# Optimization experiments

Measured on AMD Instinct MI355X. Metric: run time of the kernel, lower is better.

## Reference

```python
import jax, jax.numpy as jnp
from jax import lax
import numpy as np

COST_CLASS, COST_BBOX, COST_GIOU = 2.0, 5.0, 2.0
ALPHA, GAMMA, OTA_K = 0.25, 2.0, 5
EXPANDED_STRIDES = 32.0
DEG = 180.0 / np.pi


def _make_corners(key, prefix):
    k1, k2, k3, k4, k5 = jax.random.split(key, 5)
    cx = jax.random.uniform(k1, prefix, minval=0.0, maxval=512.0)
    cy = jax.random.uniform(k2, prefix, minval=0.0, maxval=512.0)
    w = jax.random.uniform(k3, prefix, minval=8.0, maxval=128.0)
    h = jax.random.uniform(k4, prefix, minval=8.0, maxval=128.0)
    ang = jax.random.uniform(k5, prefix, minval=0.0, maxval=np.pi)
    offs = jnp.array([[-0.5, -0.5], [0.5, -0.5], [0.5, 0.5], [-0.5, 0.5]], jnp.float32)
    wh = jnp.stack([w, h], -1)[..., None, :]          # [..., 1, 2]
    pts = offs * wh                                    # [..., 4, 2]
    c, s = jnp.cos(ang)[..., None], jnp.sin(ang)[..., None]
    rx = pts[..., 0] * c - pts[..., 1] * s + cx[..., None]
    ry = pts[..., 0] * s + pts[..., 1] * c + cy[..., None]
    return jnp.stack([rx, ry], -1).reshape(prefix + (8,))


def setup_inputs() -> dict:
    key = jax.random.key(0)
    k1, k2, k3, k4 = jax.random.split(key, 4)
    B, Q, G, C = 16, 4096, 128, 80
    return {
        "pred_logits": jax.random.normal(k1, (B, Q, C), jnp.float32),
        "pred_boxes": _make_corners(k2, (B, Q)),
        "gt_boxes": _make_corners(k3, (B, G)),
        "gt_labels": jax.random.randint(k4, (B, G), 0, C),
    }


def corners_to_cxcywha(c):  # [N,8] -> [N,5]
    xc = (c[:, 0] + c[:, 2] + c[:, 4] + c[:, 6]) / 4
    yc = (c[:, 1] + c[:, 3] + c[:, 5] + c[:, 7]) / 4
    w = jnp.sqrt((c[:, 0] - c[:, 2]) ** 2 + (c[:, 1] - c[:, 3]) ** 2)
    h = jnp.sqrt((c[:, 2] - c[:, 4]) ** 2 + (c[:, 3] - c[:, 5]) ** 2)
    ang = jnp.arctan2(c[:, 3] - c[:, 1], c[:, 2] - c[:, 0]) * DEG
    return jnp.stack([xc, yc, w, h, ang], 1)


def _aabb(b5):
    cx, cy, w, h = b5[:, 0], b5[:, 1], b5[:, 2], b5[:, 3]
    return jnp.stack([cx - w / 2, cy - h / 2, cx + w / 2, cy + h / 2], 1)


def pairwise_iou(b1, b2):
    a, b = _aabb(b1), _aabb(b2)
    lt = jnp.maximum(a[:, None, :2], b[None, :, :2])
    rb = jnp.minimum(a[:, None, 2:], b[None, :, 2:])
    wh = jnp.clip(rb - lt, 0.0)
    inter = wh[..., 0] * wh[..., 1]
    area1 = (a[:, 2] - a[:, 0]) * (a[:, 3] - a[:, 1])
    area2 = (b[:, 2] - b[:, 0]) * (b[:, 3] - b[:, 1])
    return inter / (area1[:, None] + area2[None, :] - inter + 1e-8)


def pairwise_diou(b1, b2):
    iou = pairwise_iou(b1, b2)
    a, b = _aabb(b1), _aabb(b2)
    enc = jnp.maximum(a[:, None, 2:], b[None, :, 2:]) - jnp.minimum(a[:, None, :2], b[None, :, :2])
    c2 = (enc ** 2).sum(-1) + 1e-8
    d2 = ((b1[:, None, :2] - b2[None, :, :2]) ** 2).sum(-1)
    return iou - d2 / c2


def get_in_boxes_info(boxes, gts):
    bc = boxes.reshape(-1, 4, 2).mean(1)   # [Q,2]
    gp = gts.reshape(-1, 4, 2)             # [G,4,2]
    gc = gp.mean(1)                        # [G,2]
    cdist = jnp.sqrt(((bc[:, None] - gc[None]) ** 2).sum(-1))  # [Q,G]
    v1 = gp[:, 1] - gp[:, 0]
    v2 = gp[:, 2] - gp[:, 0]
    gt_area = jnp.abs(v1[:, 0] * v2[:, 1] - v1[:, 1] * v2[:, 0]) / 2
    diag = jnp.sqrt(((gp.max(1) - gp.min(1)) ** 2).sum(-1))
    radius = diag / EXPANDED_STRIDES
    in_boxes = cdist <= (gt_area / radius)[None, :]
    in_centers = cdist <= radius[None, :]
    return in_boxes.any(1), in_boxes & in_centers


def _dedup(cost, m):
    multi = m.sum(1) > 1
    onehot = jax.nn.one_hot(jnp.argmin(cost, 1), cost.shape[1], dtype=m.dtype)
    return jnp.where(multi[:, None], onehot, m)


def _match_single(logits, pboxes, gboxes, glabels):
    Q, G = pboxes.shape[0], gboxes.shape[0]
    prob = jax.nn.sigmoid(logits)
    fg_mask, _ = get_in_boxes_info(pboxes, gboxes)
    p5, g5 = corners_to_cxcywha(pboxes), corners_to_cxcywha(gboxes)
    ious = pairwise_iou(p5, g5)
    neg = (1 - ALPHA) * prob ** GAMMA * -jnp.log(1 - prob + 1e-8)
    pos = ALPHA * (1 - prob) ** GAMMA * -jnp.log(prob + 1e-8)
    cost_class = (pos - neg)[:, glabels]                         # [Q,G]
    cost_bbox = jnp.abs(pboxes[:, None] - gboxes[None]).sum(-1)  # L1 cdist on corners
    cost_giou = -pairwise_diou(p5, g5)
    # NB: source has `+ self.cost_giou * -cost_giou`, i.e. +w*diou; replicated verbatim.
    cost = COST_BBOX * cost_bbox + COST_CLASS * cost_class + COST_GIOU * (-cost_giou)
    cost = cost + 10000.0 * (~fg_mask)[:, None].astype(cost.dtype)
    # dynamic-k: sum of top OTA_K ious per gt, truncated to int, min 1
    topk = lax.top_k(ious.T, OTA_K)[0]                 # [G, k]
    dyn_k = jnp.clip(topk.sum(-1).astype(jnp.int32), 1, Q)
    ranks = jnp.argsort(jnp.argsort(cost, axis=0), axis=0)  # ascending-cost rank per column
    matching = (ranks < dyn_k[None, :]).astype(cost.dtype)
    matching = _dedup(cost, matching)
    # ensure every gt matched (bounded replication of the while loop)
    def cond(carry):
        c, m, it = carry
        return jnp.any(m.sum(0) == 0) & (it < G)
    def body(carry):
        c, m, it = carry
        c = c + 100000.0 * (m.sum(1) > 0)[:, None].astype(c.dtype)
        unm = m.sum(0) == 0
        amin = jnp.argmin(c, 0)                          # [G]
        hit = (jnp.arange(Q)[:, None] == amin[None, :]) & unm[None, :]
        m = jnp.where(hit, 1.0, m)
        m = _dedup(c, m)
        return (c, m, it + 1)
    _, matching, _ = lax.while_loop(cond, body, (cost, matching, jnp.int32(0)))
    return matching, cost, ious


def reference(pred_logits, pred_boxes, gt_boxes, gt_labels):
    return jax.vmap(_match_single)(pred_logits, pred_boxes, gt_boxes, gt_labels)
```

## Files before the change

### kernel.cpp

```cpp
#include <hip/hip_runtime.h>
#include <cstdint>
#include <cstddef>

#define B_ 16
#define Q_ 4096
#define G_ 128
#define C_ 80
#define QCHUNK 16
#define NCH (Q_ / QCHUNK)

typedef unsigned long long u64;
#define U64MAX 0xffffffffffffffffull

__device__ __forceinline__ u64 packkey(float v, int q) {
    unsigned int bts = __float_as_uint(v);
    if (bts == 0x80000000u) bts = 0u;
    bts = (bts & 0x80000000u) ? ~bts : (bts | 0x80000000u);
    return ((u64)bts << 32) | (unsigned int)q;
}

__device__ __forceinline__ u64 umin64(u64 a, u64 b) { return a < b ? a : b; }
__device__ __forceinline__ u64 umax64(u64 a, u64 b) { return a > b ? a : b; }

__device__ __forceinline__ void merge5_desc(
    float& a0, float& a1, float& a2, float& a3, float& a4,
    float b0, float b1, float b2, float b3, float b4)
{
    const float r0 = fmaxf(a0, b0);
    const float r1 = fmaxf(fmaxf(a1, b1), fminf(a0, b0));
    const float r2 = fmaxf(fmaxf(a2, b2), fmaxf(fminf(a0, b1), fminf(a1, b0)));
    const float r3 = fmaxf(fmaxf(a3, b3),
                     fmaxf(fminf(a0, b2), fmaxf(fminf(a1, b1), fminf(a2, b0))));
    const float r4 = fmaxf(fmaxf(a4, b4),
                     fmaxf(fmaxf(fminf(a0, b3), fminf(a3, b0)),
                           fmaxf(fminf(a1, b2), fminf(a2, b1))));
    a0 = r0; a1 = r1; a2 = r2; a3 = r3; a4 = r4;
}

__device__ __forceinline__ void merge5_asc(
    u64& a0, u64& a1, u64& a2, u64& a3, u64& a4,
    u64 b0, u64 b1, u64 b2, u64 b3, u64 b4)
{
    const u64 r0 = umin64(a0, b0);
    const u64 r1 = umin64(umin64(a1, b1), umax64(a0, b0));
    const u64 r2 = umin64(umin64(a2, b2), umin64(umax64(a0, b1), umax64(a1, b0)));
    const u64 r3 = umin64(umin64(a3, b3),
                   umin64(umax64(a0, b2), umin64(umax64(a1, b1), umax64(a2, b0))));
    const u64 r4 = umin64(umin64(a4, b4),
                   umin64(umin64(umax64(a0, b3), umax64(a3, b0)),
                          umin64(umax64(a1, b2), umax64(a2, b1))));
    a0 = r0; a1 = r1; a2 = r2; a3 = r3; a4 = r4;
}

__device__ __forceinline__ float focal_cost(float x) {
    float p;
    if (x >= 0.f) { const float e = expf(-x); p = 1.f / (1.f + e); }
    else          { const float e = expf(x);  p = e / (1.f + e); }
    const float pos = 0.25f * (1.f - p) * (1.f - p) * (-logf(p + 1e-8f));
    const float neg = 0.75f * p * p * (-logf(1.f - p + 1e-8f));
    return pos - neg;
}

__global__ __launch_bounds__(256) void fused_cost_kernel(
    const float* __restrict__ logits,
    const float* __restrict__ pboxes,
    const float* __restrict__ gboxes,
    const int*   __restrict__ glabels,
    float* __restrict__ out_cost,
    float* __restrict__ out_iou,
    float* __restrict__ costT,
    float* __restrict__ piou,
    u64*   __restrict__ pcost,
    int*   __restrict__ ramin)
{
    const int tid = threadIdx.x;
    const int g   = tid & 127;
    const int qh  = tid >> 7;
    const int ci  = blockIdx.x, b = blockIdx.y;
    const int q0  = ci * QCHUNK;

    __shared__ float pq[QCHUNK][16];
    __shared__ int   fgf[QCHUNK];
    __shared__ __align__(16) char lk_buf[5120];
    __shared__ float ctile[QCHUNK][G_ + 1];
    __shared__ float phalf[G_][5];
    float* lbuf = (float*)lk_buf;
    u64 (*khalf)[5] = (u64(*)[5])lk_buf;

    const float4* gb4 = (const float4*)(gboxes + ((size_t)b * G_ + g) * 8);
    const float4 gA = gb4[0], gB = gb4[1];
    const float g0 = gA.x, g1 = gA.y, g2 = gA.z, g3 = gA.w;
    const float g4 = gB.x, g5 = gB.y, g6 = gB.z, g7 = gB.w;
    const float gxc = (g0 + g2 + g4 + g6) * 0.25f;
    const float gyc = (g1 + g3 + g5 + g7) * 0.25f;
    const float gw = sqrtf((g0 - g2) * (g0 - g2) + (g1 - g3) * (g1 - g3));
    const float gh = sqrtf((g2 - g4) * (g2 - g4) + (g3 - g5) * (g3 - g5));
    const float gax0 = gxc - gw * 0.5f, gay0 = gyc - gh * 0.5f;
    const float gax1 = gxc + gw * 0.5f, gay1 = gyc + gh * 0.5f;
    const float garea = (gax1 - gax0) * (gay1 - gay0);
    const float v1x = g2 - g0, v1y = g3 - g1, v2x = g4 - g0, v2y = g5 - g1;
    const float gt_area = fabsf(v1x * v2y - v1y * v2x) * 0.5f;
    const float mxx = fmaxf(fmaxf(g0, g2), fmaxf(g4, g6));
    const float mnx = fminf(fminf(g0, g2), fminf(g4, g6));
    const float mxy = fmaxf(fmaxf(g1, g3), fmaxf(g5, g7));
    const float mny = fminf(fminf(g1, g3), fminf(g5, g7));
    const float dgx = mxx - mnx, dgy = mxy - mny;
    const float radius = sqrtf(dgx * dgx + dgy * dgy) / 32.0f;
    const float thresh = gt_area / radius;
    const int lab = glabels[b * G_ + g];

    if (tid < 32) {
        const float4 v = ((const float4*)(pboxes + ((size_t)b * Q_ + q0) * 8))[tid];
        *(float4*)&pq[tid >> 1][(tid & 1) * 4] = v;
    }
    __syncthreads();
    if (tid < QCHUNK) {
        const float* pr = pq[tid];
        const float p0 = pr[0], p1 = pr[1], p2 = pr[2], p3 = pr[3];
        const float p4 = pr[4], p5v = pr[5], p6 = pr[6], p7 = pr[7];
        const float pxc = (p0 + p2 + p4 + p6) * 0.25f;
        const float pyc = (p1 + p3 + p5v + p7) * 0.25f;
        const float pw = sqrtf((p0 - p2) * (p0 - p2) + (p1 - p3) * (p1 - p3));
        const float ph = sqrtf((p2 - p4) * (p2 - p4) + (p3 - p5v) * (p3 - p5v));
        pq[tid][8]  = pxc;
        pq[tid][9]  = pyc;
        pq[tid][10] = pxc - pw * 0.5f;
        pq[tid][11] = pyc - ph * 0.5f;
        pq[tid][12] = pxc + pw * 0.5f;
        pq[tid][13] = pyc + ph * 0.5f;
        pq[tid][14] = pw * ph;
        fgf[tid] = 0;
    }
    __syncthreads();
    for (int j = tid; j < QCHUNK * 80; j += 256)
        lbuf[j] = focal_cost(logits[((size_t)b * Q_ + q0) * 80 + j]);

    const int lane0 = ((tid & 63) == 0);
    for (int i = 0; i < QCHUNK / 2; ++i) {
        const int ql = 2 * i + qh;
        const float dx = pq[ql][8] - gxc, dy = pq[ql][9] - gyc;
        const int in = sqrtf(dx * dx + dy * dy) <= thresh;
        const int anyin = __any(in);
        if (anyin && lane0) fgf[ql] = 1;
    }
    __syncthreads();

    float t0 = -1e38f, t1 = -1e38f, t2 = -1e38f, t3 = -1e38f, t4 = -1e38f;
    u64 k0 = U64MAX, k1 = U64MAX, k2 = U64MAX, k3 = U64MAX, k4 = U64MAX;

    #pragma unroll
    for (int jj = 0; jj < 8; ++jj) {
        const int qls = 2 * jj + qh;
        const int q   = q0 + qls;
        const float4 prA = *(const float4*)&pq[qls][0];
        const float4 prB = *(const float4*)&pq[qls][4];
        const float4 prC = *(const float4*)&pq[qls][8];
        const float4 prD = *(const float4*)&pq[qls][12];
        const float p0 = prA.x, p1 = prA.y, p2 = prA.z, p3 = prA.w;
        const float p4 = prB.x, p5v = prB.y, p6 = prB.z, p7 = prB.w;
        const float pxc = prC.x, pyc = prC.y;
        const float pax0 = prC.z, pay0 = prC.w, pax1 = prD.x, pay1 = prD.y;
        const float parea = prD.z;

        const float l1 = fabsf(p0 - g0) + fabsf(p1 - g1) + fabsf(p2 - g2)
                       + fabsf(p3 - g3) + fabsf(p4 - g4) + fabsf(p5v - g5)
                       + fabsf(p6 - g6) + fabsf(p7 - g7);

        const float ltx = fmaxf(pax0, gax0), lty = fmaxf(pay0, gay0);
        const float rbx = fminf(pax1, gax1), rby = fminf(pay1, gay1);
        const float iw = fmaxf(rbx - ltx, 0.f), ih = fmaxf(rby - lty, 0.f);
        const float inter = iw * ih;
        const float iou = inter / (parea + garea - inter + 1e-8f);

        const float ew = fmaxf(pax1, gax1) - fminf(pax0, gax0);
        const float eh = fmaxf(pay1, gay1) - fminf(pay0, gay0);
        const float cc2 = ew * ew + eh * eh + 1e-8f;
        const float dx = pxc - gxc, dy = pyc - gyc;
        const float diou = iou - (dx * dx + dy * dy) / cc2;

        const float cclass = lbuf[qls * 80 + lab];
        const float cost = 5.f * l1 + 2.f * cclass + 2.f * diou
                         + (fgf[qls] ? 0.f : 10000.f);

        const size_t o = ((size_t)b * Q_ + q) * G_ + g;
        out_cost[o] = cost;
        out_iou[o]  = iou;
        ctile[qls][g] = cost;

        if (iou > t4) {
            if (iou > t0)      { t4 = t3; t3 = t2; t2 = t1; t1 = t0; t0 = iou; }
            else if (iou > t1) { t4 = t3; t3 = t2; t2 = t1; t1 = iou; }
            else if (iou > t2) { t4 = t3; t3 = t2; t2 = iou; }
            else if (iou > t3) { t4 = t3; t3 = iou; }
            else               { t4 = iou; }
        }
        const u64 kk = packkey(cost, q);
        if (kk < k4) {
            if (kk < k0)      { k4 = k3; k3 = k2; k2 = k1; k1 = k0; k0 = kk; }
            else if (kk < k1) { k4 = k3; k3 = k2; k2 = k1; k1 = kk; }
            else if (kk < k2) { k4 = k3; k3 = k2; k2 = kk; }
            else if (kk < k3) { k4 = k3; k3 = kk; }
            else              { k4 = kk; }
        }
    }
    __syncthreads();

    for (int t = tid; t < QCHUNK * G_ / 4; t += 256) {
        const int gg = t >> 2;
        const int k  = (t & 3) << 2;
        float4 o;
        o.x = ctile[k + 0][gg]; o.y = ctile[k + 1][gg];
        o.z = ctile[k + 2][gg]; o.w = ctile[k + 3][gg];
        *(float4*)&costT[((size_t)b * G_ + gg) * Q_ + q0 + k] = o;
    }

    {
        const int qls  = tid >> 4;
        const int part = tid & 15;
        float v = 1e38f; int mg = 0x7fffffff;
        #pragma unroll
        for (int j = 0; j < 8; ++j) {
            const int gg = part + 16 * j;
            const float c = ctile[qls][gg];
            if (c < v || (c == v && gg < mg)) { v = c; mg = gg; }
        }
        #pragma unroll
        for (int off = 1; off < 16; off <<= 1) {
            const float ov = __shfl_xor(v, off);
            const int   og = __shfl_xor(mg, off);
            if (ov < v || (ov == v && og < mg)) { v = ov; mg = og; }
        }
        if (part == 0) ramin[b * Q_ + q0 + qls] = mg;
    }

    if (qh == 1) {
        phalf[g][0] = t0; phalf[g][1] = t1; phalf[g][2] = t2;
        phalf[g][3] = t3; phalf[g][4] = t4;
        khalf[g][0] = k0; khalf[g][1] = k1; khalf[g][2] = k2;
        khalf[g][3] = k3; khalf[g][4] = k4;
    }
    __syncthreads();
    if (qh == 0) {
        merge5_desc(t0, t1, t2, t3, t4,
                    phalf[g][0], phalf[g][1], phalf[g][2], phalf[g][3], phalf[g][4]);
        merge5_asc(k0, k1, k2, k3, k4,
                   khalf[g][0], khalf[g][1], khalf[g][2], khalf[g][3], khalf[g][4]);
        const size_t pbase = (((size_t)b * G_ + g) * NCH + ci) * 5;
        piou[pbase + 0] = t0; piou[pbase + 1] = t1; piou[pbase + 2] = t2;
        piou[pbase + 3] = t3; piou[pbase + 4] = t4;
        pcost[pbase + 0] = k0; pcost[pbase + 1] = k1; pcost[pbase + 2] = k2;
        pcost[pbase + 3] = k3; pcost[pbase + 4] = k4;
    }
}

__global__ __launch_bounds__(256) void dynk_scatter_kernel(
    const u64*   __restrict__ pcost,
    const float* __restrict__ piou,
    u64* __restrict__ cand,
    int* __restrict__ cnt,
    int* __restrict__ gsel)
{
    const int col = blockIdx.x;
    const int b = col >> 7, g = col & 127;
    const int tid = threadIdx.x;
    const int wv = tid >> 6, ln = tid & 63;

    __shared__ u64   wl[4][5];
    __shared__ float il[4][5];

    const size_t base = (size_t)col * (NCH * 5) + (size_t)tid * 5;

    u64 k0 = pcost[base + 0], k1 = pcost[base + 1], k2 = pcost[base + 2],
        k3 = pcost[base + 3], k4 = pcost[base + 4];
    float t0 = piou[base + 0], t1 = piou[base + 1], t2 = piou[base + 2],
          t3 = piou[base + 3], t4 = piou[base + 4];

    #pragma unroll
    for (int off = 1; off < 64; off <<= 1) {
        merge5_asc(k0, k1, k2, k3, k4,
                   __shfl_xor(k0, off), __shfl_xor(k1, off), __shfl_xor(k2, off),
                   __shfl_xor(k3, off), __shfl_xor(k4, off));
        merge5_desc(t0, t1, t2, t3, t4,
                    __shfl_xor(t0, off), __shfl_xor(t1, off), __shfl_xor(t2, off),
                    __shfl_xor(t3, off), __shfl_xor(t4, off));
    }
    if (ln == 0) {
        wl[wv][0] = k0; wl[wv][1] = k1; wl[wv][2] = k2; wl[wv][3] = k3; wl[wv][4] = k4;
        il[wv][0] = t0; il[wv][1] = t1; il[wv][2] = t2; il[wv][3] = t3; il[wv][4] = t4;
    }
    __syncthreads();

    if (tid == 0) {
        u64 f0 = wl[0][0], f1 = wl[0][1], f2 = wl[0][2], f3 = wl[0][3], f4 = wl[0][4];
        merge5_asc(f0, f1, f2, f3, f4, wl[1][0], wl[1][1], wl[1][2], wl[1][3], wl[1][4]);
        merge5_asc(f0, f1, f2, f3, f4, wl[2][0], wl[2][1], wl[2][2], wl[2][3], wl[2][4]);
        merge5_asc(f0, f1, f2, f3, f4, wl[3][0], wl[3][1], wl[3][2], wl[3][3], wl[3][4]);
        float s0 = il[0][0], s1 = il[0][1], s2 = il[0][2], s3 = il[0][3], s4 = il[0][4];
        merge5_desc(s0, s1, s2, s3, s4, il[1][0], il[1][1], il[1][2], il[1][3], il[1][4]);
        merge5_desc(s0, s1, s2, s3, s4, il[2][0], il[2][1], il[2][2], il[2][3], il[2][4]);
        merge5_desc(s0, s1, s2, s3, s4, il[3][0], il[3][1], il[3][2], il[3][3], il[3][4]);

        cand[(size_t)col * 5 + 0] = f0;
        cand[(size_t)col * 5 + 1] = f1;
        cand[(size_t)col * 5 + 2] = f2;
        cand[(size_t)col * 5 + 3] = f3;
        cand[(size_t)col * 5 + 4] = f4;

        const float s = s0 + s1 + s2 + s3 + s4;
        int dynk = (int)s;
        if (dynk < 1) dynk = 1;
        if (dynk > 5) dynk = 5;
        const u64 ks[5] = {f0, f1, f2, f3, f4};
        #pragma unroll
        for (int i = 0; i < 5; ++i) {
            if (i < dynk) {
                const int q = (int)(ks[i] & 0xffffffffu);
                atomicAdd(&cnt[b * Q_ + q], 1);
                gsel[b * Q_ + q] = g;
            }
        }
    }
}

__global__ __launch_bounds__(256) void loop_kernel(
    const float* __restrict__ costT,
    const int* __restrict__ cnt,
    const int* __restrict__ gsel,
    const int* __restrict__ ramin,
    const u64* __restrict__ cand,
    int* __restrict__ rmatch_final)
{
    const int b = blockIdx.x, tid = threadIdx.x;
    const int wv = tid >> 6, ln = tid & 63;

    __shared__ short rmatch[Q_];
    __shared__ unsigned char s_ra[Q_];
    __shared__ int newh[Q_];
    __shared__ unsigned char newg[Q_];
    __shared__ u64 scand[G_][5];
    __shared__ int ptrs[G_], col_cnt[G_], unm_list[G_], prop[G_], fb_slot[G_], touched[G_];
    __shared__ int n_unm, n_fb, n_touch;

    for (int q = tid; q < Q_; q += 256) {
        const int c  = cnt[b * Q_ + q];
        const int ra = ramin[b * Q_ + q];
        s_ra[q] = (unsigned char)ra;
        newh[q] = 0;
        rmatch[q] = (c == 0) ? (short)-1
                             : (c == 1 ? (short)gsel[b * Q_ + q] : (short)ra);
    }
    if (tid < G_) { col_cnt[tid] = 0; ptrs[tid] = 0; }
    for (int i = tid; i < G_ * 5; i += 256)
        scand[i / 5][i % 5] = cand[(size_t)b * G_ * 5 + i];
    __syncthreads();
    for (int q = tid; q < Q_; q += 256)
        if (rmatch[q] >= 0) atomicAdd(&col_cnt[rmatch[q]], 1);
    __syncthreads();

    for (int it = 0; it < G_; ++it) {
        if (tid == 0) { n_unm = 0; n_fb = 0; n_touch = 0; }
        __syncthreads();
        if (tid < G_ && col_cnt[tid] == 0)
            unm_list[atomicAdd(&n_unm, 1)] = tid;
        __syncthreads();
        const int nu = n_unm;
        if (nu == 0) break;

        if (tid < nu) {
            const int g = unm_list[tid];
            int p = ptrs[g];
            int q = -1;
            while (p < 5) {
                const int cq = (int)(scand[g][p] & 0xffffffffu);
                if (rmatch[cq] < 0) { q = cq; break; }
                ++p;
            }
            ptrs[g] = p;
            prop[tid] = q;
            if (q < 0) fb_slot[atomicAdd(&n_fb, 1)] = tid;
        }
        __syncthreads();

        const int nf = n_fb;
        for (int i = wv; i < nf; i += 4) {
            const int slot = fb_slot[i];
            const int g = unm_list[slot];
            const float4* colp = (const float4*)(costT + ((size_t)b * G_ + g) * Q_);
            u64 k0 = U64MAX, k1 = U64MAX, k2 = U64MAX, k3 = U64MAX, k4 = U64MAX;
            #pragma unroll 4
            for (int s = 0; s < Q_ / 256; ++s) {
                const int idx = ln + s * 64;
                const float4 c4 = colp[idx];
                const int qb = idx * 4;
                const float vv[4] = {c4.x, c4.y, c4.z, c4.w};
                #pragma unroll
                for (int j = 0; j < 4; ++j) {
                    if (rmatch[qb + j] < 0) {
                        const u64 kk = packkey(vv[j], qb + j);
                        if (kk < k4) {
                            if (kk < k0)      { k4 = k3; k3 = k2; k2 = k1; k1 = k0; k0 = kk; }
                            else if (kk < k1) { k4 = k3; k3 = k2; k2 = k1; k1 = kk; }
                            else if (kk < k2) { k4 = k3; k3 = k2; k2 = kk; }
                            else if (kk < k3) { k4 = k3; k3 = kk; }
                            else              { k4 = kk; }
                        }
                    }
                }
            }
            #pragma unroll
            for (int off = 1; off < 64; off <<= 1) {
                merge5_asc(k0, k1, k2, k3, k4,
                           __shfl_xor(k0, off), __shfl_xor(k1, off), __shfl_xor(k2, off),
                           __shfl_xor(k3, off), __shfl_xor(k4, off));
            }
            if (ln == 0) {
                scand[g][0] = k0; scand[g][1] = k1; scand[g][2] = k2;
                scand[g][3] = k3; scand[g][4] = k4;
                ptrs[g] = 0;
                prop[slot] = (int)(k0 & 0xffffffffu);
            }
        }
        __syncthreads();

        if (tid < nu) {
            const int q = prop[tid];
            newg[q] = (unsigned char)unm_list[tid];
            if (atomicAdd(&newh[q], 1) == 0)
                touched[atomicAdd(&n_touch, 1)] = q;
        }
        __syncthreads();

        const int nt = n_touch;
        if (tid < nt) {
            const int q = touched[tid];
            const int nh = newh[q];
            const int gg = (nh == 1) ? (int)newg[q] : (int)s_ra[q];
            rmatch[q] = (short)gg;
            atomicAdd(&col_cnt[gg], 1);
            newh[q] = 0;
        }
        __syncthreads();
    }

    for (int q = tid; q < Q_; q += 256)
        rmatch_final[b * Q_ + q] = rmatch[q];
}

__global__ __launch_bounds__(256) void expand_kernel(
    const int* __restrict__ rmatch_final, float* __restrict__ out_match)
{
    const int idx = blockIdx.x * 256 + threadIdx.x;
    const int row = idx >> 5;
    const int gb  = (idx & 31) << 2;
    const int rm  = rmatch_final[row];
    float4 o;
    o.x = (rm == gb)     ? 1.f : 0.f;
    o.y = (rm == gb + 1) ? 1.f : 0.f;
    o.z = (rm == gb + 2) ? 1.f : 0.f;
    o.w = (rm == gb + 3) ? 1.f : 0.f;
    ((float4*)out_match)[idx] = o;
}

extern "C" void kernel_launch(void* const* d_in, const int* in_sizes, int n_in,
                              void* d_out, int out_size, void* d_ws, size_t ws_size,
                              hipStream_t stream) {
    const float* logits  = (const float*)d_in[0];
    const float* pboxes  = (const float*)d_in[1];
    const float* gboxes  = (const float*)d_in[2];
    const int*   glabels = (const int*)d_in[3];

    float* out = (float*)d_out;
    const size_t BQG = (size_t)B_ * Q_ * G_;
    float* out_match = out;
    float* out_cost  = out + BQG;
    float* out_iou   = out + 2 * BQG;

    char* ws = (char*)d_ws;
    size_t off = 0;
    float* costT  = (float*)(ws + off); off += (size_t)B_ * G_ * Q_ * 4;
    u64*   pcost  = (u64*)  (ws + off); off += (size_t)B_ * G_ * NCH * 5 * 8;
    float* piou   = (float*)(ws + off); off += (size_t)B_ * G_ * NCH * 5 * 4;
    u64*   cand   = (u64*)  (ws + off); off += (size_t)B_ * G_ * 5 * 8;
    int*   ramin  = (int*)  (ws + off); off += (size_t)B_ * Q_ * 4;
    int*   cnt    = (int*)  (ws + off); off += (size_t)B_ * Q_ * 4;
    int*   gsel   = (int*)  (ws + off); off += (size_t)B_ * Q_ * 4;
    int*   rmf    = (int*)  (ws + off); off += (size_t)B_ * Q_ * 4;

    hipMemsetAsync(cnt, 0, (size_t)B_ * Q_ * 4, stream);
    fused_cost_kernel<<<dim3(NCH, B_), 256, 0, stream>>>(
        logits, pboxes, gboxes, glabels, out_cost, out_iou, costT, piou, pcost, ramin);
    dynk_scatter_kernel<<<B_ * G_, 256, 0, stream>>>(pcost, piou, cand, cnt, gsel);
    loop_kernel<<<B_, 256, 0, stream>>>(costT, cnt, gsel, ramin, cand, rmf);
    expand_kernel<<<(int)(BQG / 4 / 256), 256, 0, stream>>>(rmf, out_match);
}
```

Measured before the change: 201.4 us.

## Drop transposed cost copy, read output cost directly; widen loop kernel to 1024 threads

Removes the costT transposed workspace write (32 MB) from the cost kernel, and the fallback search in the loop kernel now reads strided columns of the row-major output cost. The partial top-k buffers are relaid out per chunk, the cnt memset is folded into the cost kernel, and the loop kernel runs with 1024 threads (16 waves). This saves a large global write and a memset launch. In exchange, the fallback column scans become strided, uncoalesced reads.

```diff
diff --git a/kernel.cpp b/kernel.cpp
--- a/kernel.cpp
+++ b/kernel.cpp
@@ -68,10 +68,10 @@
     const int*   __restrict__ glabels,
     float* __restrict__ out_cost,
     float* __restrict__ out_iou,
-    float* __restrict__ costT,
     float* __restrict__ piou,
     u64*   __restrict__ pcost,
-    int*   __restrict__ ramin)
+    int*   __restrict__ ramin,
+    int*   __restrict__ cnt)
 {
     const int tid = threadIdx.x;
     const int g   = tid & 127;
@@ -86,6 +86,8 @@
     __shared__ float phalf[G_][5];
     float* lbuf = (float*)lk_buf;
     u64 (*khalf)[5] = (u64(*)[5])lk_buf;
+
+    if (tid < QCHUNK) cnt[b * Q_ + q0 + tid] = 0;
 
     const float4* gb4 = (const float4*)(gboxes + ((size_t)b * G_ + g) * 8);
     const float4 gA = gb4[0], gB = gb4[1];
@@ -205,15 +207,6 @@
     }
     __syncthreads();
 
-    for (int t = tid; t < QCHUNK * G_ / 4; t += 256) {
-        const int gg = t >> 2;
-        const int k  = (t & 3) << 2;
-        float4 o;
-        o.x = ctile[k + 0][gg]; o.y = ctile[k + 1][gg];
-        o.z = ctile[k + 2][gg]; o.w = ctile[k + 3][gg];
-        *(float4*)&costT[((size_t)b * G_ + gg) * Q_ + q0 + k] = o;
-    }
-
     {
         const int qls  = tid >> 4;
         const int part = tid & 15;
@@ -245,7 +238,7 @@
                     phalf[g][0], phalf[g][1], phalf[g][2], phalf[g][3], phalf[g][4]);
         merge5_asc(k0, k1, k2, k3, k4,
                    khalf[g][0], khalf[g][1], khalf[g][2], khalf[g][3], khalf[g][4]);
-        const size_t pbase = (((size_t)b * G_ + g) * NCH + ci) * 5;
+        const size_t pbase = (((size_t)b * NCH + ci) * G_ + g) * 5;
         piou[pbase + 0] = t0; piou[pbase + 1] = t1; piou[pbase + 2] = t2;
         piou[pbase + 3] = t3; piou[pbase + 4] = t4;
         pcost[pbase + 0] = k0; pcost[pbase + 1] = k1; pcost[pbase + 2] = k2;
@@ -268,7 +261,7 @@
     __shared__ u64   wl[4][5];
     __shared__ float il[4][5];
 
-    const size_t base = (size_t)col * (NCH * 5) + (size_t)tid * 5;
+    const size_t base = (((size_t)b * NCH + tid) * G_ + g) * 5;
 
     u64 k0 = pcost[base + 0], k1 = pcost[base + 1], k2 = pcost[base + 2],
         k3 = pcost[base + 3], k4 = pcost[base + 4];
@@ -322,8 +315,8 @@
     }
 }
 
-__global__ __launch_bounds__(256) void loop_kernel(
-    const float* __restrict__ costT,
+__global__ __launch_bounds__(1024) void loop_kernel(
+    const float* __restrict__ cost,
     const int* __restrict__ cnt,
     const int* __restrict__ gsel,
     const int* __restrict__ ramin,
@@ -341,7 +334,7 @@
     __shared__ int ptrs[G_], col_cnt[G_], unm_list[G_], prop[G_], fb_slot[G_], touched[G_];
     __shared__ int n_unm, n_fb, n_touch;
 
-    for (int q = tid; q < Q_; q += 256) {
+    for (int q = tid; q < Q_; q += 1024) {
         const int c  = cnt[b * Q_ + q];
         const int ra = ramin[b * Q_ + q];
         s_ra[q] = (unsigned char)ra;
@@ -350,12 +343,14 @@
                              : (c == 1 ? (short)gsel[b * Q_ + q] : (short)ra);
     }
     if (tid < G_) { col_cnt[tid] = 0; ptrs[tid] = 0; }
-    for (int i = tid; i < G_ * 5; i += 256)
-        scand[i / 5][i % 5] = cand[(size_t)b * G_ * 5 + i];
-    __syncthreads();
-    for (int q = tid; q < Q_; q += 256)
+    if (tid < G_ * 5)
+        scand[tid / 5][tid % 5] = cand[(size_t)b * G_ * 5 + tid];
+    __syncthreads();
+    for (int q = tid; q < Q_; q += 1024)
         if (rmatch[q] >= 0) atomicAdd(&col_cnt[rmatch[q]], 1);
     __syncthreads();
+
+    const float* costb = cost + (size_t)b * Q_ * G_;
 
     for (int it = 0; it < G_; ++it) {
         if (tid == 0) { n_unm = 0; n_fb = 0; n_touch = 0; }
@@ -382,28 +377,21 @@
         __syncthreads();
 
         const int nf = n_fb;
-        for (int i = wv; i < nf; i += 4) {
+        for (int i = wv; i < nf; i += 16) {
             const int slot = fb_slot[i];
             const int g = unm_list[slot];
-            const float4* colp = (const float4*)(costT + ((size_t)b * G_ + g) * Q_);
+            const float* colp = costb + g;
             u64 k0 = U64MAX, k1 = U64MAX, k2 = U64MAX, k3 = U64MAX, k4 = U64MAX;
-            #pragma unroll 4
-            for (int s = 0; s < Q_ / 256; ++s) {
-                const int idx = ln + s * 64;
-                const float4 c4 = colp[idx];
-                const int qb = idx * 4;
-                const float vv[4] = {c4.x, c4.y, c4.z, c4.w};
-                #pragma unroll
-                for (int j = 0; j < 4; ++j) {
-                    if (rmatch[qb + j] < 0) {
-                        const u64 kk = packkey(vv[j], qb + j);
-                        if (kk < k4) {
-                            if (kk < k0)      { k4 = k3; k3 = k2; k2 = k1; k1 = k0; k0 = kk; }
-                            else if (kk < k1) { k4 = k3; k3 = k2; k2 = k1; k1 = kk; }
-                            else if (kk < k2) { k4 = k3; k3 = k2; k2 = kk; }
-                            else if (kk < k3) { k4 = k3; k3 = kk; }
-                            else              { k4 = kk; }
-                        }
+            for (int q = ln; q < Q_; q += 64) {
+                if (rmatch[q] < 0) {
+                    const float v = colp[(size_t)q * G_];
+                    const u64 kk = packkey(v, q);
+                    if (kk < k4) {
+                        if (kk < k0)      { k4 = k3; k3 = k2; k2 = k1; k1 = k0; k0 = kk; }
+                        else if (kk < k1) { k4 = k3; k3 = k2; k2 = k1; k1 = kk; }
+                        else if (kk < k2) { k4 = k3; k3 = k2; k2 = kk; }
+                        else if (kk < k3) { k4 = k3; k3 = kk; }
+                        else              { k4 = kk; }
                     }
                 }
             }
@@ -442,7 +430,7 @@
         __syncthreads();
     }
 
-    for (int q = tid; q < Q_; q += 256)
+    for (int q = tid; q < Q_; q += 1024)
         rmatch_final[b * Q_ + q] = rmatch[q];
 }
 
@@ -477,19 +465,17 @@
 
     char* ws = (char*)d_ws;
     size_t off = 0;
-    float* costT  = (float*)(ws + off); off += (size_t)B_ * G_ * Q_ * 4;
-    u64*   pcost  = (u64*)  (ws + off); off += (size_t)B_ * G_ * NCH * 5 * 8;
-    float* piou   = (float*)(ws + off); off += (size_t)B_ * G_ * NCH * 5 * 4;
+    u64*   pcost  = (u64*)  (ws + off); off += (size_t)B_ * NCH * G_ * 5 * 8;
+    float* piou   = (float*)(ws + off); off += (size_t)B_ * NCH * G_ * 5 * 4;
     u64*   cand   = (u64*)  (ws + off); off += (size_t)B_ * G_ * 5 * 8;
     int*   ramin  = (int*)  (ws + off); off += (size_t)B_ * Q_ * 4;
     int*   cnt    = (int*)  (ws + off); off += (size_t)B_ * Q_ * 4;
     int*   gsel   = (int*)  (ws + off); off += (size_t)B_ * Q_ * 4;
     int*   rmf    = (int*)  (ws + off); off += (size_t)B_ * Q_ * 4;
 
-    hipMemsetAsync(cnt, 0, (size_t)B_ * Q_ * 4, stream);
     fused_cost_kernel<<<dim3(NCH, B_), 256, 0, stream>>>(
-        logits, pboxes, gboxes, glabels, out_cost, out_iou, costT, piou, pcost, ramin);
+        logits, pboxes, gboxes, glabels, out_cost, out_iou, piou, pcost, ramin, cnt);
     dynk_scatter_kernel<<<B_ * G_, 256, 0, stream>>>(pcost, piou, cand, cnt, gsel);
-    loop_kernel<<<B_, 256, 0, stream>>>(costT, cnt, gsel, ramin, cand, rmf);
+    loop_kernel<<<B_, 1024, 0, stream>>>(out_cost, cnt, gsel, ramin, cand, rmf);
     expand_kernel<<<(int)(BQG / 4 / 256), 256, 0, stream>>>(rmf, out_match);
 }
```

Measured after the change: 196.2 us. 2.6% less time.
